# Optimization experiments

Hardware: AMD Instinct MI355X
Metric: run time of the kernel (lower is better)

The kernel has to match this reference:

```python
import jax, jax.numpy as jnp
import numpy as np

LN_EPS = 1e-12
B, L, D, V, PATCH, IMG, C = 64, 40, 768, 30522, 16, 384, 3
GRID = IMG // PATCH            # 24
NPATCH = GRID * GRID           # 576


def layer_norm(x, g, b):
    m = jnp.mean(x, axis=-1, keepdims=True)
    v = jnp.var(x, axis=-1, keepdims=True)
    return (x - m) * jax.lax.rsqrt(v + LN_EPS) * g + b


def setup_inputs() -> dict:
    key = jax.random.key(0)
    ks = jax.random.split(key, 12)
    s = 0.02
    return {
        "input_ids": jax.random.randint(ks[0], (B, L), 0, V, dtype=jnp.int32),
        "attention_mask": jnp.ones((B, L), jnp.int32),
        "token_type_ids": jnp.zeros((B, L), jnp.int32),
        "pixel_values": jax.random.normal(ks[1], (B, C, IMG, IMG), jnp.float32),
        "pixel_mask": jnp.ones((B, IMG, IMG), jnp.int32),
        "word_emb": jax.random.normal(ks[2], (V, D), jnp.float32) * s,
        "text_pos_emb": jax.random.normal(ks[3], (L, D), jnp.float32) * s,
        "text_tok_emb": jax.random.normal(ks[4], (2, D), jnp.float32) * s,
        "ln_g": jnp.ones((D,), jnp.float32),
        "ln_b": jnp.zeros((D,), jnp.float32),
        "conv_w": jax.random.normal(ks[5], (D, C, PATCH, PATCH), jnp.float32) * s,
        "conv_b": jnp.zeros((D,), jnp.float32),
        "cls_token": jnp.zeros((1, 1, D), jnp.float32),
        "vis_pos_emb": jax.random.normal(ks[6], (1, NPATCH + 1, D), jnp.float32) * s,
        "mod_type_emb": jax.random.normal(ks[7], (2, D), jnp.float32) * s,
    }


def reference(input_ids, attention_mask, token_type_ids, pixel_values, pixel_mask,
              word_emb, text_pos_emb, text_tok_emb, ln_g, ln_b,
              conv_w, conv_b, cls_token, vis_pos_emb, mod_type_emb):
    # ---- text embeddings (BERT-style) ----
    te = word_emb[input_ids] + text_pos_emb[None, :, :] + text_tok_emb[token_type_ids]
    te = layer_norm(te, ln_g, ln_b)  # [B, L, D]

    # ---- visual_embed ----
    # patch projection conv (stride = patch size)
    x = jax.lax.conv_general_dilated(
        pixel_values, conv_w, window_strides=(PATCH, PATCH), padding='VALID',
        dimension_numbers=('NCHW', 'OIHW', 'NCHW')) + conv_b[None, :, None, None]
    # [B, D, 24, 24] -> [B, 576, D]
    x = x.reshape(B, D, NPATCH).transpose(0, 2, 1)
    # full pixel_mask => x_h = x_w = GRID for every sample; bilinear interp of the
    # [1, D, 24, 24] spatial pos-embed to (24, 24) with align_corners=True is identity,
    # all patches valid, valid_nums == max_image_length => selection is identity.
    pos_embed = vis_pos_emb[:, 1:, :]           # [1, NPATCH, D]
    img = x + pos_embed                          # [B, NPATCH, D]
    image_masks = jnp.ones((B, NPATCH), attention_mask.dtype)

    # ---- modality type embeddings ----
    te = te + mod_type_emb[0][None, None, :]
    img = img + mod_type_emb[1][None, None, :]

    # ---- concat with cls token ----
    emb = jnp.concatenate([te, img], axis=1)
    cls = jnp.broadcast_to(cls_token, (B, 1, D))
    emb = jnp.concatenate([cls, emb], axis=1)    # [B, 1+L+NPATCH, D]
    masks = jnp.concatenate(
        [jnp.ones((B, 1), attention_mask.dtype), attention_mask, image_masks], axis=1)
    return emb, masks
```

## Files before the change

### kernel.cpp

```cpp
#include <hip/hip_runtime.h>

typedef __attribute__((ext_vector_type(4))) float f4;
typedef __attribute__((ext_vector_type(4))) float f32x4;
typedef __attribute__((ext_vector_type(8))) __bf16 bf8;
typedef __attribute__((ext_vector_type(8))) unsigned short us8;

#define NB 64
#define LSEQ 40
#define D_DIM 768
#define NPATCH 576
#define SEQ 617
#define K_DIM 768
#define M_DIM (NB * NPATCH)
#define GEMM_LDS 131072

static __device__ __forceinline__ unsigned short f2bf(float f) {
    union { float f; unsigned u; } v; v.f = f;
    unsigned r = v.u + 0x7FFFu + ((v.u >> 16) & 1u);
    return (unsigned short)(r >> 16);
}

static __device__ __forceinline__ void gload_lds16(const void* g, void* l) {
    __builtin_amdgcn_global_load_lds(
        (const __attribute__((address_space(1))) unsigned int*)g,
        (__attribute__((address_space(3))) unsigned int*)l,
        16, 0, 0);
}

#define MFMA16(a, b, c) __builtin_amdgcn_mfma_f32_16x16x32_bf16((a), (b), (c), 0, 0, 0)

__global__ __launch_bounds__(256) void convert_w(const float* __restrict__ w,
                                                 unsigned short* __restrict__ o) {
    int t = blockIdx.x * 256 + threadIdx.x;
    int cs = t % 96, n = t / 96;
    int blk = cs >> 3, c = cs & 7;
    int cl = (blk << 3) | (c ^ (n & 7));
    const float* s = w + (size_t)n * 768 + cl * 8;
    f4 a = *(const f4*)s;
    f4 b = *(const f4*)(s + 4);
    us8 r;
    r[0]=f2bf(a[0]); r[1]=f2bf(a[1]); r[2]=f2bf(a[2]); r[3]=f2bf(a[3]);
    r[4]=f2bf(b[0]); r[5]=f2bf(b[1]); r[6]=f2bf(b[2]); r[7]=f2bf(b[3]);
    *(us8*)(o + (size_t)n * 768 + cs * 8) = r;
}

__global__ __launch_bounds__(256) void text_kernel(
    const int* __restrict__ ids, const int* __restrict__ tti,
    const float* __restrict__ we, const float* __restrict__ pe,
    const float* __restrict__ tke, const float* __restrict__ g,
    const float* __restrict__ bb, const float* __restrict__ mod,
    float* __restrict__ out) {
    int row = blockIdx.x * 4 + (threadIdx.x >> 6);
    int lane = threadIdx.x & 63;
    int b = row / 40, l = row % 40;
    const float* wp = we + (size_t)ids[row] * 768;
    const float* pp = pe + l * 768;
    const float* tp = tke + (size_t)tti[row] * 768;
    f4 x[3];
    float s = 0.f, q = 0.f;
#pragma unroll
    for (int j = 0; j < 3; ++j) {
        int d = j * 256 + lane * 4;
        f4 v = *(const f4*)(wp + d);
        f4 v2 = *(const f4*)(pp + d);
        f4 v3 = *(const f4*)(tp + d);
        v = v + v2 + v3;
        x[j] = v;
        s += v[0] + v[1] + v[2] + v[3];
        q += v[0]*v[0] + v[1]*v[1] + v[2]*v[2] + v[3]*v[3];
    }
#pragma unroll
    for (int o = 32; o > 0; o >>= 1) { s += __shfl_xor(s, o); q += __shfl_xor(q, o); }
    float mean = s * (1.0f / 768.0f);
    float var = q * (1.0f / 768.0f) - mean * mean;
    float rstd = rsqrtf(var + 1e-12f);
    float* op = out + ((size_t)b * SEQ + 1 + l) * 768;
#pragma unroll
    for (int j = 0; j < 3; ++j) {
        int d = j * 256 + lane * 4;
        f4 gg = *(const f4*)(g + d);
        f4 bv = *(const f4*)(bb + d);
        f4 mm = *(const f4*)(mod + d);
        f4 r = (x[j] - mean) * rstd * gg + bv + mm;
        *(f4*)(op + d) = r;
    }
}

__global__ __launch_bounds__(512, 2) void gemm_patch(
    const float* __restrict__ px, const __bf16* __restrict__ W,
    const float* __restrict__ conv_b, const float* __restrict__ vis_pos,
    const float* __restrict__ mod, float* __restrict__ out) {
    extern __shared__ __align__(16) char smem[];
    char* Ab0 = smem;
    char* Ab1 = smem + 32768;
    char* Bb0 = smem + 65536;
    char* Bb1 = smem + 98304;

    const int tid = threadIdx.x;
    const int w = tid >> 6, lane = tid & 63;

    int lid = blockIdx.x;
    int gwi = (lid & 7) * 54 + (lid >> 3);
    const int tile_n = (gwi % 3) * 256;
    const int tile_m = (gwi / 3) * 256;
    const int wm = w >> 2, wn = w & 3;
    const int wr = wm * 128, wc = wn * 64;

    f32x4 acc[8][4] = {};
    const char* Bb = (const char*)W;
    const int rsel = lane & 15;
    const int hk = lane >> 4;

    const int arow = tid & 255;
    const int ii0 = tid >> 8;
    {
    }
    int agm = tile_m + arow;
    int abimg = agm / 576, ap = agm % 576;
    int aph = ap / 24, apw = ap % 24;
    const float* pxrow = px + (size_t)abimg * 3 * 147456
                            + (size_t)(aph * 16) * 384 + apw * 16;

    f4 areg[2][4];
    auto LOAD_A = [&](int kt) {
        int c = kt >> 2, i0 = (kt & 3) << 2;
#pragma unroll
        for (int rep = 0; rep < 2; ++rep) {
            int i = i0 + ii0 + rep * 2;
            const float* s = pxrow + (size_t)c * 147456 + i * 384;
#pragma unroll
            for (int q = 0; q < 4; ++q) areg[rep][q] = *(const f4*)(s + q * 4);
        }
    };
    auto WRITE_A = [&](char* dst) {
#pragma unroll
        for (int rep = 0; rep < 2; ++rep) {
            int ii = ii0 + rep * 2;
            us8 h0, h1;
#pragma unroll
            for (int q = 0; q < 2; ++q) {
                h0[q*4+0]=f2bf(areg[rep][q][0]); h0[q*4+1]=f2bf(areg[rep][q][1]);
                h0[q*4+2]=f2bf(areg[rep][q][2]); h0[q*4+3]=f2bf(areg[rep][q][3]);
                h1[q*4+0]=f2bf(areg[rep][q+2][0]); h1[q*4+1]=f2bf(areg[rep][q+2][1]);
                h1[q*4+2]=f2bf(areg[rep][q+2][2]); h1[q*4+3]=f2bf(areg[rep][q+2][3]);
            }
            int cc0 = ii * 2;
            *(us8*)(dst + arow * 128 + ((cc0    ) ^ (arow & 7)) * 16) = h0;
            *(us8*)(dst + arow * 128 + ((cc0 + 1) ^ (arow & 7)) * 16) = h1;
        }
    };
    auto STAGE_B = [&](char* lbase, int kt) {
#pragma unroll
        for (int i = 0; i < 4; ++i) {
            int uoff = (w << 10) + i * 8192;
            int loff = uoff + (lane << 4);
            int row = loff >> 7, col = loff & 127;
            gload_lds16(Bb + (size_t)(tile_n + row) * 1536 + kt * 128 + col,
                        lbase + uoff);
        }
    };

    LOAD_A(0);
    STAGE_B(Bb0, 0);
    WRITE_A(Ab0);
    __syncthreads();

    for (int t = 0; t < 12; ++t) {
        char* Ac = (t & 1) ? Ab1 : Ab0;
        char* Bc = (t & 1) ? Bb1 : Bb0;
        char* An = (t & 1) ? Ab0 : Ab1;
        char* Bn = (t & 1) ? Bb0 : Bb1;

        if (t < 11) {
            LOAD_A(t + 1);
            STAGE_B(Bn, t + 1);
        }

        bf8 a0[4][2], b0[4][2];
#pragma unroll
        for (int mi = 0; mi < 4; ++mi) {
            int r = wr + mi * 16 + rsel;
#pragma unroll
            for (int ks = 0; ks < 2; ++ks) {
                int cst = (ks * 4 + hk) ^ (r & 7);
                a0[mi][ks] = *(const bf8*)(Ac + r * 128 + cst * 16);
            }
        }
#pragma unroll
        for (int ni = 0; ni < 4; ++ni) {
            int r = wc + ni * 16 + rsel;
#pragma unroll
            for (int ks = 0; ks < 2; ++ks) {
                int cst = (ks * 4 + hk) ^ (r & 7);
                b0[ni][ks] = *(const bf8*)(Bc + r * 128 + cst * 16);
            }
        }
#pragma unroll
        for (int mi = 0; mi < 4; ++mi)
#pragma unroll
            for (int ni = 0; ni < 4; ++ni) {
                acc[mi][ni] = MFMA16(a0[mi][0], b0[ni][0], acc[mi][ni]);
                acc[mi][ni] = MFMA16(a0[mi][1], b0[ni][1], acc[mi][ni]);
            }

        bf8 a1[4][2];
#pragma unroll
        for (int mi = 0; mi < 4; ++mi) {
            int r = wr + 64 + mi * 16 + rsel;
#pragma unroll
            for (int ks = 0; ks < 2; ++ks) {
                int cst = (ks * 4 + hk) ^ (r & 7);
                a1[mi][ks] = *(const bf8*)(Ac + r * 128 + cst * 16);
            }
        }
#pragma unroll
        for (int mi = 0; mi < 4; ++mi)
#pragma unroll
            for (int ni = 0; ni < 4; ++ni) {
                acc[4 + mi][ni] = MFMA16(a1[mi][0], b0[ni][0], acc[4 + mi][ni]);
                acc[4 + mi][ni] = MFMA16(a1[mi][1], b0[ni][1], acc[4 + mi][ni]);
            }

        if (t < 11) {
            WRITE_A(An);
            __syncthreads();
        }
    }

    const int lr = (lane >> 4) * 4;
    const int lc = lane & 15;
#pragma unroll
    for (int mi = 0; mi < 8; ++mi) {
#pragma unroll
        for (int r = 0; r < 4; ++r) {
            int gm = tile_m + wr + mi * 16 + lr + r;
            int bimg = gm / 576, pp2 = gm % 576;
            size_t orow = (size_t)bimg * SEQ + 1 + LSEQ + pp2;
#pragma unroll
            for (int ni = 0; ni < 4; ++ni) {
                int gn = tile_n + wc + ni * 16 + lc;
                float v = acc[mi][ni][r] + conv_b[gn] +
                          vis_pos[(size_t)(pp2 + 1) * 768 + gn] + mod[768 + gn];
                out[orow * 768 + gn] = v;
            }
        }
    }
}

__global__ __launch_bounds__(256) void cls_masks(const float* __restrict__ cls,
                                                 const int* __restrict__ am,
                                                 float* __restrict__ out) {
    int t = blockIdx.x * 256 + threadIdx.x;
    if (t < NB * 768) {
        int b = t / 768, d = t % 768;
        out[(size_t)b * SEQ * 768 + d] = cls[d];
    } else if (t < NB * 768 + NB * SEQ) {
        int i = t - NB * 768;
        int b = i / SEQ, s = i % SEQ;
        float v = 1.0f;
        if (s >= 1 && s <= LSEQ) v = (float)am[b * LSEQ + s - 1];
        out[(size_t)NB * SEQ * 768 + i] = v;
    }
}

extern "C" void kernel_launch(void* const* d_in, const int* in_sizes, int n_in,
                              void* d_out, int out_size, void* d_ws, size_t ws_size,
                              hipStream_t stream) {
    const int*   ids  = (const int*)d_in[0];
    const int*   am   = (const int*)d_in[1];
    const int*   tti  = (const int*)d_in[2];
    const float* px   = (const float*)d_in[3];
    const float* we   = (const float*)d_in[5];
    const float* pe   = (const float*)d_in[6];
    const float* tke  = (const float*)d_in[7];
    const float* lng  = (const float*)d_in[8];
    const float* lnb  = (const float*)d_in[9];
    const float* cw   = (const float*)d_in[10];
    const float* cb   = (const float*)d_in[11];
    const float* cls  = (const float*)d_in[12];
    const float* vpos = (const float*)d_in[13];
    const float* mod  = (const float*)d_in[14];
    float* out = (float*)d_out;

    __bf16* Wbf = (__bf16*)d_ws;

    hipFuncSetAttribute((const void*)gemm_patch,
                        hipFuncAttributeMaxDynamicSharedMemorySize, GEMM_LDS);

    convert_w<<<288, 256, 0, stream>>>(cw, (unsigned short*)Wbf);
    text_kernel<<<640, 256, 0, stream>>>(ids, tti, we, pe, tke, lng, lnb, mod, out);
    gemm_patch<<<432, 512, GEMM_LDS, stream>>>(px, Wbf, cb, vpos, mod, out);
    cls_masks<<<347, 256, 0, stream>>>(cls, am, out);
}
```

Before: 101.5 us.

## Deepen A-operand prefetch to two tiles and merge cls/mask kernel into text kernel

After: 220.9 us. 118% more time.

```diff
diff --git a/kernel.cpp b/kernel.cpp
--- a/kernel.cpp
+++ b/kernel.cpp
@@ -44,45 +44,61 @@
     *(us8*)(o + (size_t)n * 768 + cs * 8) = r;
 }
 
-__global__ __launch_bounds__(256) void text_kernel(
+__global__ __launch_bounds__(256) void text_cls_kernel(
     const int* __restrict__ ids, const int* __restrict__ tti,
     const float* __restrict__ we, const float* __restrict__ pe,
     const float* __restrict__ tke, const float* __restrict__ g,
     const float* __restrict__ bb, const float* __restrict__ mod,
+    const float* __restrict__ cls, const int* __restrict__ am,
     float* __restrict__ out) {
-    int row = blockIdx.x * 4 + (threadIdx.x >> 6);
-    int lane = threadIdx.x & 63;
-    int b = row / 40, l = row % 40;
-    const float* wp = we + (size_t)ids[row] * 768;
-    const float* pp = pe + l * 768;
-    const float* tp = tke + (size_t)tti[row] * 768;
-    f4 x[3];
-    float s = 0.f, q = 0.f;
-#pragma unroll
-    for (int j = 0; j < 3; ++j) {
-        int d = j * 256 + lane * 4;
-        f4 v = *(const f4*)(wp + d);
-        f4 v2 = *(const f4*)(pp + d);
-        f4 v3 = *(const f4*)(tp + d);
-        v = v + v2 + v3;
-        x[j] = v;
-        s += v[0] + v[1] + v[2] + v[3];
-        q += v[0]*v[0] + v[1]*v[1] + v[2]*v[2] + v[3]*v[3];
-    }
-#pragma unroll
-    for (int o = 32; o > 0; o >>= 1) { s += __shfl_xor(s, o); q += __shfl_xor(q, o); }
-    float mean = s * (1.0f / 768.0f);
-    float var = q * (1.0f / 768.0f) - mean * mean;
-    float rstd = rsqrtf(var + 1e-12f);
-    float* op = out + ((size_t)b * SEQ + 1 + l) * 768;
-#pragma unroll
-    for (int j = 0; j < 3; ++j) {
-        int d = j * 256 + lane * 4;
-        f4 gg = *(const f4*)(g + d);
-        f4 bv = *(const f4*)(bb + d);
-        f4 mm = *(const f4*)(mod + d);
-        f4 r = (x[j] - mean) * rstd * gg + bv + mm;
-        *(f4*)(op + d) = r;
+    int blk = blockIdx.x;
+    if (blk < 640) {
+        int row = blk * 4 + (threadIdx.x >> 6);
+        int lane = threadIdx.x & 63;
+        int b = row / 40, l = row % 40;
+        const float* wp = we + (size_t)ids[row] * 768;
+        const float* pp = pe + l * 768;
+        const float* tp = tke + (size_t)tti[row] * 768;
+        f4 x[3];
+        float s = 0.f, q = 0.f;
+#pragma unroll
+        for (int j = 0; j < 3; ++j) {
+            int d = j * 256 + lane * 4;
+            f4 v = *(const f4*)(wp + d);
+            f4 v2 = *(const f4*)(pp + d);
+            f4 v3 = *(const f4*)(tp + d);
+            v = v + v2 + v3;
+            x[j] = v;
+            s += v[0] + v[1] + v[2] + v[3];
+            q += v[0]*v[0] + v[1]*v[1] + v[2]*v[2] + v[3]*v[3];
+        }
+#pragma unroll
+        for (int o = 32; o > 0; o >>= 1) { s += __shfl_xor(s, o); q += __shfl_xor(q, o); }
+        float mean = s * (1.0f / 768.0f);
+        float var = q * (1.0f / 768.0f) - mean * mean;
+        float rstd = rsqrtf(var + 1e-12f);
+        float* op = out + ((size_t)b * SEQ + 1 + l) * 768;
+#pragma unroll
+        for (int j = 0; j < 3; ++j) {
+            int d = j * 256 + lane * 4;
+            f4 gg = *(const f4*)(g + d);
+            f4 bv = *(const f4*)(bb + d);
+            f4 mm = *(const f4*)(mod + d);
+            f4 r = (x[j] - mean) * rstd * gg + bv + mm;
+            *(f4*)(op + d) = r;
+        }
+    } else {
+        int t = (blk - 640) * 256 + threadIdx.x;
+        if (t < NB * 768) {
+            int b = t / 768, d = t % 768;
+            out[(size_t)b * SEQ * 768 + d] = cls[d];
+        } else if (t < NB * 768 + NB * SEQ) {
+            int i = t - NB * 768;
+            int b = i / SEQ, s = i % SEQ;
+            float v = 1.0f;
+            if (s >= 1 && s <= LSEQ) v = (float)am[b * LSEQ + s - 1];
+            out[(size_t)NB * SEQ * 768 + i] = v;
+        }
     }
 }
 
@@ -113,42 +129,45 @@
 
     const int arow = tid & 255;
     const int ii0 = tid >> 8;
-    {
-    }
     int agm = tile_m + arow;
     int abimg = agm / 576, ap = agm % 576;
     int aph = ap / 24, apw = ap % 24;
     const float* pxrow = px + (size_t)abimg * 3 * 147456
                             + (size_t)(aph * 16) * 384 + apw * 16;
 
-    f4 areg[2][4];
-    auto LOAD_A = [&](int kt) {
-        int c = kt >> 2, i0 = (kt & 3) << 2;
-#pragma unroll
-        for (int rep = 0; rep < 2; ++rep) {
-            int i = i0 + ii0 + rep * 2;
-            const float* s = pxrow + (size_t)c * 147456 + i * 384;
-#pragma unroll
-            for (int q = 0; q < 4; ++q) areg[rep][q] = *(const f4*)(s + q * 4);
-        }
-    };
-    auto WRITE_A = [&](char* dst) {
-#pragma unroll
-        for (int rep = 0; rep < 2; ++rep) {
-            int ii = ii0 + rep * 2;
-            us8 h0, h1;
-#pragma unroll
-            for (int q = 0; q < 2; ++q) {
-                h0[q*4+0]=f2bf(areg[rep][q][0]); h0[q*4+1]=f2bf(areg[rep][q][1]);
-                h0[q*4+2]=f2bf(areg[rep][q][2]); h0[q*4+3]=f2bf(areg[rep][q][3]);
-                h1[q*4+0]=f2bf(areg[rep][q+2][0]); h1[q*4+1]=f2bf(areg[rep][q+2][1]);
-                h1[q*4+2]=f2bf(areg[rep][q+2][2]); h1[q*4+3]=f2bf(areg[rep][q+2][3]);
-            }
-            int cc0 = ii * 2;
-            *(us8*)(dst + arow * 128 + ((cc0    ) ^ (arow & 7)) * 16) = h0;
-            *(us8*)(dst + arow * 128 + ((cc0 + 1) ^ (arow & 7)) * 16) = h1;
-        }
-    };
+    f4 aregA[2][4], aregB[2][4];
+
+#define LOAD_A(REG, kt)                                                      \
+    {                                                                        \
+        int c = (kt) >> 2, i0 = ((kt) & 3) << 2;                             \
+        _Pragma("unroll")                                                    \
+        for (int rep = 0; rep < 2; ++rep) {                                  \
+            int i = i0 + ii0 + rep * 2;                                      \
+            const float* s = pxrow + (size_t)c * 147456 + i * 384;           \
+            _Pragma("unroll")                                                \
+            for (int q = 0; q < 4; ++q) REG[rep][q] = *(const f4*)(s + q*4); \
+        }                                                                    \
+    }
+
+#define WRITE_A(REG, dst)                                                    \
+    {                                                                        \
+        _Pragma("unroll")                                                    \
+        for (int rep = 0; rep < 2; ++rep) {                                  \
+            int ii = ii0 + rep * 2;                                          \
+            us8 h0, h1;                                                      \
+            _Pragma("unroll")                                                \
+            for (int q = 0; q < 2; ++q) {                                    \
+                h0[q*4+0]=f2bf(REG[rep][q][0]); h0[q*4+1]=f2bf(REG[rep][q][1]); \
+                h0[q*4+2]=f2bf(REG[rep][q][2]); h0[q*4+3]=f2bf(REG[rep][q][3]); \
+                h1[q*4+0]=f2bf(REG[rep][q+2][0]); h1[q*4+1]=f2bf(REG[rep][q+2][1]); \
+                h1[q*4+2]=f2bf(REG[rep][q+2][2]); h1[q*4+3]=f2bf(REG[rep][q+2][3]); \
+            }                                                                \
+            int cc0 = ii * 2;                                                \
+            *(us8*)((dst) + arow * 128 + ((cc0    ) ^ (arow & 7)) * 16) = h0;\
+            *(us8*)((dst) + arow * 128 + ((cc0 + 1) ^ (arow & 7)) * 16) = h1;\
+        }                                                                    \
+    }
+
     auto STAGE_B = [&](char* lbase, int kt) {
 #pragma unroll
         for (int i = 0; i < 4; ++i) {
@@ -160,72 +179,81 @@
         }
     };
 
-    LOAD_A(0);
     STAGE_B(Bb0, 0);
-    WRITE_A(Ab0);
-    __syncthreads();
-
-    for (int t = 0; t < 12; ++t) {
-        char* Ac = (t & 1) ? Ab1 : Ab0;
-        char* Bc = (t & 1) ? Bb1 : Bb0;
-        char* An = (t & 1) ? Ab0 : Ab1;
-        char* Bn = (t & 1) ? Bb0 : Bb1;
-
-        if (t < 11) {
-            LOAD_A(t + 1);
-            STAGE_B(Bn, t + 1);
-        }
-
-        bf8 a0[4][2], b0[4][2];
-#pragma unroll
-        for (int mi = 0; mi < 4; ++mi) {
-            int r = wr + mi * 16 + rsel;
-#pragma unroll
-            for (int ks = 0; ks < 2; ++ks) {
-                int cst = (ks * 4 + hk) ^ (r & 7);
-                a0[mi][ks] = *(const bf8*)(Ac + r * 128 + cst * 16);
-            }
-        }
-#pragma unroll
-        for (int ni = 0; ni < 4; ++ni) {
-            int r = wc + ni * 16 + rsel;
-#pragma unroll
-            for (int ks = 0; ks < 2; ++ks) {
-                int cst = (ks * 4 + hk) ^ (r & 7);
-                b0[ni][ks] = *(const bf8*)(Bc + r * 128 + cst * 16);
-            }
-        }
-#pragma unroll
-        for (int mi = 0; mi < 4; ++mi)
-#pragma unroll
-            for (int ni = 0; ni < 4; ++ni) {
-                acc[mi][ni] = MFMA16(a0[mi][0], b0[ni][0], acc[mi][ni]);
-                acc[mi][ni] = MFMA16(a0[mi][1], b0[ni][1], acc[mi][ni]);
-            }
-
-        bf8 a1[4][2];
-#pragma unroll
-        for (int mi = 0; mi < 4; ++mi) {
-            int r = wr + 64 + mi * 16 + rsel;
-#pragma unroll
-            for (int ks = 0; ks < 2; ++ks) {
-                int cst = (ks * 4 + hk) ^ (r & 7);
-                a1[mi][ks] = *(const bf8*)(Ac + r * 128 + cst * 16);
-            }
-        }
-#pragma unroll
-        for (int mi = 0; mi < 4; ++mi)
-#pragma unroll
-            for (int ni = 0; ni < 4; ++ni) {
-                acc[4 + mi][ni] = MFMA16(a1[mi][0], b0[ni][0], acc[4 + mi][ni]);
-                acc[4 + mi][ni] = MFMA16(a1[mi][1], b0[ni][1], acc[4 + mi][ni]);
-            }
-
-        if (t < 11) {
-            WRITE_A(An);
-            __syncthreads();
-        }
-    }
+    LOAD_A(aregA, 0);
+    LOAD_A(aregB, 1);
+    WRITE_A(aregA, Ab0);
+    asm volatile("s_waitcnt vmcnt(8) lgkmcnt(0)" ::: "memory");
+    __builtin_amdgcn_sched_barrier(0);
+    __builtin_amdgcn_s_barrier();
+    __builtin_amdgcn_sched_barrier(0);
+
+#define TILE_BODY(t, LR, WR, Ac, Bc, An, Bn)                                 \
+    {                                                                        \
+        const bool doS = (t) + 1 < 12;                                       \
+        const bool doL = (t) + 2 < 12;                                       \
+        if (doS) STAGE_B(Bn, (t) + 1);                                       \
+        if (doL) LOAD_A(LR, (t) + 2);                                        \
+        bf8 a0[4][2], b0[4][2];                                              \
+        _Pragma("unroll")                                                    \
+        for (int mi = 0; mi < 4; ++mi) {                                     \
+            int r = wr + mi * 16 + rsel;                                     \
+            _Pragma("unroll")                                                \
+            for (int ks = 0; ks < 2; ++ks) {                                 \
+                int cst = (ks * 4 + hk) ^ (r & 7);                           \
+                a0[mi][ks] = *(const bf8*)((Ac) + r * 128 + cst * 16);       \
+            }                                                                \
+        }                                                                    \
+        _Pragma("unroll")                                                    \
+        for (int ni = 0; ni < 4; ++ni) {                                     \
+            int r = wc + ni * 16 + rsel;                                     \
+            _Pragma("unroll")                                                \
+            for (int ks = 0; ks < 2; ++ks) {                                 \
+                int cst = (ks * 4 + hk) ^ (r & 7);                           \
+                b0[ni][ks] = *(const bf8*)((Bc) + r * 128 + cst * 16);       \
+            }                                                                \
+        }                                                                    \
+        if (doS) WRITE_A(WR, An);           \
+        _Pragma("unroll")                                                    \
+        for (int mi = 0; mi < 4; ++mi)                                       \
+            _Pragma("unroll")                                                \
+            for (int ni = 0; ni < 4; ++ni) {                                 \
+                acc[mi][ni] = MFMA16(a0[mi][0], b0[ni][0], acc[mi][ni]);     \
+                acc[mi][ni] = MFMA16(a0[mi][1], b0[ni][1], acc[mi][ni]);     \
+            }                                                                \
+        bf8 a1[4][2];                                                        \
+        _Pragma("unroll")                                                    \
+        for (int mi = 0; mi < 4; ++mi) {                                     \
+            int r = wr + 64 + mi * 16 + rsel;                                \
+            _Pragma("unroll")                                                \
+            for (int ks = 0; ks < 2; ++ks) {                                 \
+                int cst = (ks * 4 + hk) ^ (r & 7);                           \
+                a1[mi][ks] = *(const bf8*)((Ac) + r * 128 + cst * 16);       \
+            }                                                                \
+        }                                                                    \
+        _Pragma("unroll")                                                    \
+        for (int mi = 0; mi < 4; ++mi)                                       \
+            _Pragma("unroll")                                                \
+            for (int ni = 0; ni < 4; ++ni) {                                 \
+                acc[4+mi][ni] = MFMA16(a1[mi][0], b0[ni][0], acc[4+mi][ni]); \
+                acc[4+mi][ni] = MFMA16(a1[mi][1], b0[ni][1], acc[4+mi][ni]); \
+            }                                                                \
+        if ((t) < 11) {                                                      \
+            if (doL) { asm volatile("s_waitcnt vmcnt(8) lgkmcnt(0)" ::: "memory"); } \
+            else     { asm volatile("s_waitcnt vmcnt(0) lgkmcnt(0)" ::: "memory"); } \
+            __builtin_amdgcn_sched_barrier(0);                               \
+            __builtin_amdgcn_s_barrier();                                    \
+            __builtin_amdgcn_sched_barrier(0);                               \
+        }                                                                    \
+    }
+
+    for (int tt = 0; tt < 12; tt += 2) {
+        TILE_BODY(tt,     aregA, aregB, Ab0, Bb0, Ab1, Bb1)
+        TILE_BODY(tt + 1, aregB, aregA, Ab1, Bb1, Ab0, Bb0)
+    }
+#undef TILE_BODY
+#undef LOAD_A
+#undef WRITE_A
 
     const int lr = (lane >> 4) * 4;
     const int lc = lane & 15;
@@ -244,22 +272,6 @@
                 out[orow * 768 + gn] = v;
             }
         }
-    }
-}
-
-__global__ __launch_bounds__(256) void cls_masks(const float* __restrict__ cls,
-                                                 const int* __restrict__ am,
-                                                 float* __restrict__ out) {
-    int t = blockIdx.x * 256 + threadIdx.x;
-    if (t < NB * 768) {
-        int b = t / 768, d = t % 768;
-        out[(size_t)b * SEQ * 768 + d] = cls[d];
-    } else if (t < NB * 768 + NB * SEQ) {
-        int i = t - NB * 768;
-        int b = i / SEQ, s = i % SEQ;
-        float v = 1.0f;
-        if (s >= 1 && s <= LSEQ) v = (float)am[b * LSEQ + s - 1];
-        out[(size_t)NB * SEQ * 768 + i] = v;
     }
 }
 
@@ -288,7 +300,7 @@
                         hipFuncAttributeMaxDynamicSharedMemorySize, GEMM_LDS);
 
     convert_w<<<288, 256, 0, stream>>>(cw, (unsigned short*)Wbf);
-    text_kernel<<<640, 256, 0, stream>>>(ids, tti, we, pe, tke, lng, lnb, mod, out);
+    text_cls_kernel<<<987, 256, 0, stream>>>(ids, tti, we, pe, tke, lng, lnb,
+                                             mod, cls, am, out);
     gemm_patch<<<432, 512, GEMM_LDS, stream>>>(px, Wbf, cb, vpos, mod, out);
-    cls_masks<<<347, 256, 0, stream>>>(cls, am, out);
-}
+}
```
